# Performance work log

Measured on AMD Instinct MI355X. Metric: run time of the kernel, lower is better.

## Reference

```python
import math
import jax, jax.numpy as jnp
import numpy as np

B, N, D = 32, 1025, 768
K, CD, TD = 64, 128, 256  # num_clusters, cluster_dim, token_dim
REG = 0.1
NUM_ITERS = 5


def setup_inputs() -> dict:
    key = jax.random.key(0)
    ks = jax.random.split(key, 8)
    x = jax.random.normal(ks[0], (B, N, D), dtype=jnp.float32)
    # Linear params (torch nn.Linear: y = x @ W.T + b; we store W already transposed as [in, out])
    Wf = jax.random.normal(ks[1], (D, CD), dtype=jnp.float32) / math.sqrt(D)
    bf = jnp.zeros((CD,), dtype=jnp.float32)
    Ws = jax.random.normal(ks[2], (D, K), dtype=jnp.float32) / math.sqrt(D)
    bs = jnp.zeros((K,), dtype=jnp.float32)
    Wt = jax.random.normal(ks[3], (D, TD), dtype=jnp.float32) / math.sqrt(D)
    bt = jnp.zeros((TD,), dtype=jnp.float32)
    anchors = jax.random.normal(ks[4], (K, CD), dtype=jnp.float32) * 0.1
    dust_bin = jnp.float32(1.0)
    sharpness = jnp.float32(5.0)
    return {"x": x, "Wf": Wf, "bf": bf, "Ws": Ws, "bs": bs, "Wt": Wt, "bt": bt,
            "anchors": anchors, "dust_bin": dust_bin, "sharpness": sharpness}


def _log_otp_solver(log_a, log_b, M, num_iters, reg):
    M = M / reg
    u = jnp.zeros_like(log_a)  # [B, K+1]
    v = jnp.zeros_like(log_b)  # [B, N-1]
    for _ in range(num_iters):
        u = log_a - jax.nn.logsumexp(M + v[:, None, :], axis=2)
        v = log_b - jax.nn.logsumexp(M + u[:, :, None], axis=1)
    return M + u[:, :, None] + v[:, None, :]


def reference(x, Wf, bf, Ws, bs, Wt, bt, anchors, dust_bin, sharpness):
    b, n, d = x.shape
    t_global = x[:, 0]            # [B, D]
    fi = x[:, 1:]                 # [B, N-1, D]
    f = fi @ Wf + bf              # [B, N-1, CD]
    s = jnp.swapaxes(fi @ Ws + bs, 1, 2)  # [B, K, N-1]
    t = t_global @ Wt + bt        # [B, TD]
    s = s * sharpness
    dust = jnp.broadcast_to(dust_bin, (b, 1, n - 1))
    s_aug = jnp.concatenate([s, dust], axis=1)  # [B, K+1, N-1]
    log_a = jnp.full((b, K + 1), -math.log(K + 1), dtype=x.dtype)
    log_b = jnp.full((b, n - 1), -math.log(n - 1), dtype=x.dtype)
    log_P = _log_otp_solver(log_a, log_b, s_aug, NUM_ITERS, REG)
    p = jnp.exp(log_P)[:, :-1, :]  # [B, K, N-1]
    # v_agg = sum_n p[b,k,n] * (2*f[b,n,:] - anchors[k,:])  (algebraic rewrite of the broadcast sum)
    v_agg = 2.0 * jnp.einsum('bkn,bnc->bkc', p, f) - p.sum(axis=2)[:, :, None] * anchors[None]
    v_local = v_agg.reshape(b, -1)            # [B, K*CD]
    f_out = jnp.concatenate([t, v_local], axis=-1)
    norm = jnp.maximum(jnp.linalg.norm(f_out, axis=-1, keepdims=True), 1e-12)
    return f_out / norm
```

## Files before the change

kernel.cpp:

```cpp
#include <hip/hip_runtime.h>
#include <math.h>


#define BATCH 32
#define NTOK  1025
#define DIM   768
#define KDIM  64
#define CDIM  128
#define TDIM  256
#define NM1   1024
#define ROWLEN 8448
#define NITER 5
#define INV_REG 10.0f
#define NS_AGG 8
#define LOG_A (-4.17438727f)
#define LOG_B (-6.93147181f)

typedef __attribute__((ext_vector_type(8))) short short8;
typedef __attribute__((ext_vector_type(4))) float floatx4;

typedef __attribute__((address_space(3))) unsigned int lds_uint;
typedef const __attribute__((address_space(1))) unsigned int glb_uint;

__device__ __forceinline__ void gload_lds16(const void* g, void* l) {
    __builtin_amdgcn_global_load_lds((glb_uint*)g, (lds_uint*)l, 16, 0, 0);
}

__device__ __forceinline__ unsigned short bf16_rne(float f) {
    unsigned u = __builtin_bit_cast(unsigned, f);
    unsigned r = u + 0x7FFFu + ((u >> 16) & 1u);
    return (unsigned short)(r >> 16);
}

__device__ __forceinline__ short8 cvt8(float4 a, float4 b) {
    short8 r;
    r[0] = (short)bf16_rne(a.x); r[1] = (short)bf16_rne(a.y);
    r[2] = (short)bf16_rne(a.z); r[3] = (short)bf16_rne(a.w);
    r[4] = (short)bf16_rne(b.x); r[5] = (short)bf16_rne(b.y);
    r[6] = (short)bf16_rne(b.z); r[7] = (short)bf16_rne(b.w);
    return r;
}

__global__ __launch_bounds__(256) void prep(
    const float* __restrict__ Wf, const float* __restrict__ Ws,
    const float* __restrict__ bf, const float* __restrict__ bs,
    const float* __restrict__ x, const float* __restrict__ Wt,
    short* __restrict__ W_pack, float* __restrict__ bias_all,
    float* __restrict__ tpart)
{
    __shared__ float xr[256];
    const int blk = blockIdx.x, tid = threadIdx.x;
    if (blk < 576) {
        int idx = blk * 256 + tid;
        int g    = idx / 6144;
        int rem  = idx - g * 6144;
        int nf   = rem >> 9;
        int rem2 = rem & 511;
        int lane = rem2 >> 3;
        int j    = rem2 & 7;
        int k = g * 32 + (lane >> 4) * 8 + j;
        int c = nf * 16 + (lane & 15);
        float v = (c < CDIM) ? Wf[(size_t)k * CDIM + c] : Ws[(size_t)k * KDIM + (c - CDIM)];
        W_pack[idx] = (short)bf16_rne(v);
        if (idx < 192) bias_all[idx] = (idx < CDIM) ? bf[idx] : bs[idx - CDIM];
    } else {
        int i = blk - 576;
        int b = i / 3, dy = i - b * 3;
        xr[tid] = x[(size_t)b * NTOK * DIM + (size_t)dy * 256 + tid];
        __syncthreads();
        float acc = 0.f;
        const float* wp = Wt + (size_t)dy * 256 * TDIM + tid;
#pragma unroll 8
        for (int d = 0; d < 256; ++d) acc = fmaf(xr[d], wp[(size_t)d * TDIM], acc);
        tpart[((size_t)dy * BATCH + b) * TDIM + tid] = acc;
    }
}

__global__ __launch_bounds__(256, 2) void gemm_fs(
    const float* __restrict__ x, const short* __restrict__ W_pack,
    const float* __restrict__ bias_all, const float* __restrict__ sharp_p,
    unsigned short* __restrict__ fT, float* __restrict__ Mmat)
{
    __shared__ __align__(16) short Bs[12288];
    __shared__ __align__(16) short As[4096];
    const int tid  = threadIdx.x;
    const int wave = tid >> 6, lane = tid & 63;
    const int quad = lane >> 4, lrow = lane & 15;
    const int bb0   = blockIdx.x & 31;
    const int chunk = blockIdx.x >> 5;
    const int R = bb0 * 1024 + chunk * 64 + wave * 16;

    const int arow = bb0 * 1024 + chunk * 64 + (tid >> 2);
    const float* asrc = x + ((size_t)(arow >> 10) * NTOK + 1 + (arow & 1023)) * DIM + (tid & 3) * 16;
    const int r    = (tid >> 2) & 15;
    const int seg  = tid & 3;
    const int kk_w = seg >> 1;
    const int q0   = (seg & 1) * 2;
    short* adst0 = &As[(((tid >> 6) * 2 + kk_w) * 64 + q0 * 16 + r) * 8];
    short* adst1 = &As[(((tid >> 6) * 2 + kk_w) * 64 + (q0 + 1) * 16 + r) * 8];

    floatx4 acc[12];
#pragma unroll
    for (int nf = 0; nf < 12; ++nf) acc[nf] = (floatx4){0.f, 0.f, 0.f, 0.f};

    float4 g0 = *(const float4*)(asrc);
    float4 g1 = *(const float4*)(asrc + 4);
    float4 g2 = *(const float4*)(asrc + 8);
    float4 g3 = *(const float4*)(asrc + 12);

    for (int ko = 0; ko < 12; ++ko) {
        __syncthreads();
        const short* bsrc = W_pack + ko * 12288 + tid * 8;
#pragma unroll
        for (int i = 0; i < 6; ++i)
            gload_lds16(bsrc + i * 2048, &Bs[i * 2048 + tid * 8]);
        *(short8*)adst0 = cvt8(g0, g1);
        *(short8*)adst1 = cvt8(g2, g3);
        __syncthreads();
        if (ko < 11) {
            const float* ap = asrc + (ko + 1) * 64;
            g0 = *(const float4*)(ap);
            g1 = *(const float4*)(ap + 4);
            g2 = *(const float4*)(ap + 8);
            g3 = *(const float4*)(ap + 12);
            __builtin_amdgcn_sched_barrier(0);
        }
#pragma unroll
        for (int kk = 0; kk < 2; ++kk) {
            short8 af = *(const short8*)&As[((wave * 2 + kk) * 64 + lane) * 8];
#pragma unroll
            for (int nf = 0; nf < 12; ++nf) {
                short8 bf8 = *(const short8*)&Bs[((kk * 12 + nf) * 64 + lane) * 8];
                acc[nf] = __builtin_amdgcn_mfma_f32_16x16x32_bf16(af, bf8, acc[nf], 0, 0, 0);
            }
        }
    }

    const float sc = sharp_p[0] * INV_REG;
    const int bb = R >> 10;
    const int tok = (R & 1023) + quad * 4;
#pragma unroll
    for (int nf = 0; nf < 12; ++nf) {
        const int c = nf * 16 + lrow;
        const float bias = bias_all[c];
        if (nf < 8) {
            ushort4 w;
            w.x = bf16_rne(acc[nf][0] + bias);
            w.y = bf16_rne(acc[nf][1] + bias);
            w.z = bf16_rne(acc[nf][2] + bias);
            w.w = bf16_rne(acc[nf][3] + bias);
            *(ushort4*)(fT + ((size_t)bb * CDIM + c) * NM1 + tok) = w;
        } else {
            const int k = c - CDIM;
            float4 w = make_float4((acc[nf][0] + bias) * sc, (acc[nf][1] + bias) * sc,
                                   (acc[nf][2] + bias) * sc, (acc[nf][3] + bias) * sc);
            *(float4*)(Mmat + ((size_t)bb * KDIM + k) * NM1 + tok) = w;
        }
    }
}

template<bool FIRST>
__global__ __launch_bounds__(256) void sink_u(
    const float* __restrict__ Mmat, const float* __restrict__ v_in,
    const float* __restrict__ dust_p, float* __restrict__ u_out)
{
    const int b   = blockIdx.x & 31;
    const int sub = blockIdx.x >> 5;
    const int k   = sub * 4 + (threadIdx.x >> 6);
    if (k > 64) return;
    const int lane = threadIdx.x & 63;
    const float dustM = dust_p[0] * INV_REG;

    const float4* vp = (const float4*)(v_in + (size_t)b * NM1);
    float xs[16];
    if (k < 64) {
        const float4* Mp = (const float4*)(Mmat + ((size_t)b * KDIM + k) * NM1);
#pragma unroll
        for (int i = 0; i < 4; ++i) {
            float4 mv = Mp[i * 64 + lane];
            float4 vv = FIRST ? make_float4(0.f, 0.f, 0.f, 0.f) : vp[i * 64 + lane];
            xs[i * 4 + 0] = mv.x + vv.x;
            xs[i * 4 + 1] = mv.y + vv.y;
            xs[i * 4 + 2] = mv.z + vv.z;
            xs[i * 4 + 3] = mv.w + vv.w;
        }
    } else {
#pragma unroll
        for (int i = 0; i < 4; ++i) {
            float4 vv = FIRST ? make_float4(0.f, 0.f, 0.f, 0.f) : vp[i * 64 + lane];
            xs[i * 4 + 0] = dustM + vv.x;
            xs[i * 4 + 1] = dustM + vv.y;
            xs[i * 4 + 2] = dustM + vv.z;
            xs[i * 4 + 3] = dustM + vv.w;
        }
    }
    float m = xs[0];
#pragma unroll
    for (int i = 1; i < 16; ++i) m = fmaxf(m, xs[i]);
#pragma unroll
    for (int off = 1; off < 64; off <<= 1) m = fmaxf(m, __shfl_xor(m, off));
    float S = 0.f;
#pragma unroll
    for (int i = 0; i < 16; ++i) S += __expf(xs[i] - m);
#pragma unroll
    for (int off = 1; off < 64; off <<= 1) S += __shfl_xor(S, off);
    if (lane == 0) u_out[b * 65 + k] = LOG_A - (m + __logf(S));
}

__global__ __launch_bounds__(256) void sink_v(
    const float* __restrict__ Mmat, const float* __restrict__ u_in,
    const float* __restrict__ dust_p, float* __restrict__ v_out)
{
    __shared__ float us[65];
    __shared__ float2 pp[4][64];
    const int b   = blockIdx.x & 31;
    const int ns2 = blockIdx.x >> 5;
    const int tid = threadIdx.x;
    const int tok = tid & 63, kq = tid >> 6;
    const int n = ns2 * 64 + tok;
    if (tid < 65) us[tid] = u_in[b * 65 + tid];
    __syncthreads();
    const float* Mb = Mmat + ((size_t)b * KDIM + kq * 16) * NM1 + n;
    float xs[16];
#pragma unroll
    for (int kk = 0; kk < 16; ++kk) xs[kk] = Mb[(size_t)kk * NM1] + us[kq * 16 + kk];
    float m = xs[0];
#pragma unroll
    for (int kk = 1; kk < 16; ++kk) m = fmaxf(m, xs[kk]);
    float e = 0.f;
#pragma unroll
    for (int kk = 0; kk < 16; ++kk) e += __expf(xs[kk] - m);
    pp[kq][tok] = make_float2(m, e);
    __syncthreads();
    if (tid < 64) {
        const float xd = dust_p[0] * INV_REG + us[64];
        float m3 = xd;
#pragma unroll
        for (int q = 0; q < 4; ++q) m3 = fmaxf(m3, pp[q][tid].x);
        float S3 = __expf(xd - m3);
#pragma unroll
        for (int q = 0; q < 4; ++q) S3 += pp[q][tid].y * __expf(pp[q][tid].x - m3);
        v_out[(size_t)b * NM1 + ns2 * 64 + tid] = LOG_B - (m3 + __logf(S3));
    }
}

__global__ __launch_bounds__(256) void aggregate(
    const float* __restrict__ Mmat, const unsigned short* __restrict__ fT,
    const float* __restrict__ u_in, const float* __restrict__ dust_p,
    float* __restrict__ vpart, float* __restrict__ rspart)
{
    __shared__ float us[65];
    __shared__ __align__(16) float vsh[128];
    __shared__ float wv[4][128][2];
    const int b = blockIdx.x, ns = blockIdx.y;
    const int tid = threadIdx.x;
    const int wave = tid >> 6, lane = tid & 63;
    const int quad = lane >> 4, lrow = lane & 15;
    const int krow = wave * 16 + lrow;
    const float dustM = dust_p[0] * INV_REG;

    if (tid < 65) us[tid] = u_in[b * 65 + tid];
    __syncthreads();

    float mreg[32];
    {
        const float* Mrow = Mmat + ((size_t)b * KDIM + krow) * NM1 + ns * 128 + quad * 8;
#pragma unroll
        for (int s = 0; s < 4; ++s) {
            float4 a = *(const float4*)(Mrow + s * 32);
            float4 c = *(const float4*)(Mrow + s * 32 + 4);
            mreg[s*8+0]=a.x; mreg[s*8+1]=a.y; mreg[s*8+2]=a.z; mreg[s*8+3]=a.w;
            mreg[s*8+4]=c.x; mreg[s*8+5]=c.y; mreg[s*8+6]=c.z; mreg[s*8+7]=c.w;
        }
    }

    const float uk = us[krow];
#pragma unroll
    for (int s = 0; s < 4; ++s) {
#pragma unroll
        for (int j = 0; j < 8; ++j) {
            float x = mreg[s*8+j] + uk;
            float m2 = x;
            m2 = fmaxf(m2, __shfl_xor(m2, 1));
            m2 = fmaxf(m2, __shfl_xor(m2, 2));
            m2 = fmaxf(m2, __shfl_xor(m2, 4));
            m2 = fmaxf(m2, __shfl_xor(m2, 8));
            float e = __expf(x - m2);
            e += __shfl_xor(e, 1);
            e += __shfl_xor(e, 2);
            e += __shfl_xor(e, 4);
            e += __shfl_xor(e, 8);
            if (lrow == 0) {
                wv[wave][s*32 + quad*8 + j][0] = m2;
                wv[wave][s*32 + quad*8 + j][1] = e;
            }
        }
    }
    __syncthreads();
    if (tid < 128) {
        const float xd = dustM + us[64];
        float m3 = xd;
#pragma unroll
        for (int w = 0; w < 4; ++w) m3 = fmaxf(m3, wv[w][tid][0]);
        float S3 = __expf(xd - m3);
#pragma unroll
        for (int w = 0; w < 4; ++w) S3 += wv[w][tid][1] * __expf(wv[w][tid][0] - m3);
        vsh[tid] = LOG_B - (m3 + __logf(S3));
    }
    __syncthreads();

    const unsigned short* fbase = fT + ((size_t)b * CDIM + lrow) * NM1 + ns * 128 + quad * 8;
    floatx4 acc[8];
#pragma unroll
    for (int nf = 0; nf < 8; ++nf) acc[nf] = (floatx4){0.f, 0.f, 0.f, 0.f};
    float rs = 0.f;
#pragma unroll
    for (int s = 0; s < 4; ++s) {
        const int tb = s * 32 + quad * 8;
        float4 v0 = *(const float4*)&vsh[tb];
        float4 v1 = *(const float4*)&vsh[tb + 4];
        float p[8];
        p[0] = __expf(mreg[s*8+0] + uk + v0.x);
        p[1] = __expf(mreg[s*8+1] + uk + v0.y);
        p[2] = __expf(mreg[s*8+2] + uk + v0.z);
        p[3] = __expf(mreg[s*8+3] + uk + v0.w);
        p[4] = __expf(mreg[s*8+4] + uk + v1.x);
        p[5] = __expf(mreg[s*8+5] + uk + v1.y);
        p[6] = __expf(mreg[s*8+6] + uk + v1.z);
        p[7] = __expf(mreg[s*8+7] + uk + v1.w);
        short8 afrag;
#pragma unroll
        for (int j = 0; j < 8; ++j) {
            rs += p[j];
            afrag[j] = (short)bf16_rne(p[j]);
        }
#pragma unroll
        for (int nf = 0; nf < 8; ++nf) {
            short8 bfrag = *(const short8*)(fbase + (size_t)nf * 16 * NM1 + s * 32);
            acc[nf] = __builtin_amdgcn_mfma_f32_16x16x32_bf16(afrag, bfrag, acc[nf], 0, 0, 0);
        }
    }
    rs += __shfl_xor(rs, 16);
    rs += __shfl_xor(rs, 32);
    if (lane < 16) rspart[(ns * BATCH + b) * KDIM + krow] = rs;

    float* vp = vpart + (size_t)(ns * BATCH + b) * (KDIM * CDIM);
#pragma unroll
    for (int nf = 0; nf < 8; ++nf) {
        const int c = nf * 16 + lrow;
#pragma unroll
        for (int j = 0; j < 4; ++j)
            vp[(size_t)(wave * 16 + quad * 4 + j) * CDIM + c] = acc[nf][j];
    }
}

__global__ __launch_bounds__(1024) void finalize_all(
    const float* __restrict__ vpart, const float* __restrict__ rspart,
    const float* __restrict__ anchors, const float* __restrict__ tpart,
    const float* __restrict__ bt, float* __restrict__ out)
{
    __shared__ float rstot[KDIM];
    __shared__ float red[16];
    __shared__ float sc_sh;
    const int b = blockIdx.x, tid = threadIdx.x;
    const int lane = tid & 63, wave = tid >> 6;

    if (tid < KDIM) {
        float s = 0.f;
#pragma unroll
        for (int ns = 0; ns < NS_AGG; ++ns)
            s += rspart[(ns * BATCH + b) * KDIM + tid];
        rstot[tid] = s;
    }
    __syncthreads();

    const size_t e0 = (size_t)tid * 8;
    float4 s0 = make_float4(0.f, 0.f, 0.f, 0.f);
    float4 s1 = make_float4(0.f, 0.f, 0.f, 0.f);
#pragma unroll
    for (int ns = 0; ns < NS_AGG; ++ns) {
        const float* vp = vpart + (size_t)(ns * BATCH + b) * (KDIM * CDIM) + e0;
        float4 a = *(const float4*)(vp);
        float4 c = *(const float4*)(vp + 4);
        s0.x += a.x; s0.y += a.y; s0.z += a.z; s0.w += a.w;
        s1.x += c.x; s1.y += c.y; s1.z += c.z; s1.w += c.w;
    }
    const float rsv = rstot[tid >> 4];
    float4 a0 = *(const float4*)(anchors + e0);
    float4 a1 = *(const float4*)(anchors + e0 + 4);
    float4 v0, v1;
    v0.x = 2.f * s0.x - rsv * a0.x;  v0.y = 2.f * s0.y - rsv * a0.y;
    v0.z = 2.f * s0.z - rsv * a0.z;  v0.w = 2.f * s0.w - rsv * a0.w;
    v1.x = 2.f * s1.x - rsv * a1.x;  v1.y = 2.f * s1.y - rsv * a1.y;
    v1.z = 2.f * s1.z - rsv * a1.z;  v1.w = 2.f * s1.w - rsv * a1.w;
    float ss = v0.x*v0.x + v0.y*v0.y + v0.z*v0.z + v0.w*v0.w
             + v1.x*v1.x + v1.y*v1.y + v1.z*v1.z + v1.w*v1.w;

    float t = 0.f;
    if (tid < TDIM) {
        t = bt[tid];
#pragma unroll
        for (int s = 0; s < 3; ++s) t += tpart[((size_t)s * BATCH + b) * TDIM + tid];
        ss += t * t;
    }

#pragma unroll
    for (int off = 32; off > 0; off >>= 1) ss += __shfl_down(ss, off);
    if (lane == 0) red[wave] = ss;
    __syncthreads();
    if (tid == 0) {
        float tot = 0.f;
#pragma unroll
        for (int i = 0; i < 16; ++i) tot += red[i];
        sc_sh = 1.f / fmaxf(sqrtf(tot), 1e-12f);
    }
    __syncthreads();
    const float scale = sc_sh;

    float* orow = out + (size_t)b * ROWLEN;
    if (tid < TDIM) orow[tid] = t * scale;
    v0.x *= scale; v0.y *= scale; v0.z *= scale; v0.w *= scale;
    v1.x *= scale; v1.y *= scale; v1.z *= scale; v1.w *= scale;
    *(float4*)&orow[TDIM + e0]     = v0;
    *(float4*)&orow[TDIM + e0 + 4] = v1;
}

extern "C" void kernel_launch(void* const* d_in, const int* in_sizes, int n_in,
                              void* d_out, int out_size, void* d_ws, size_t ws_size,
                              hipStream_t stream)
{
    const float* x       = (const float*)d_in[0];
    const float* Wf      = (const float*)d_in[1];
    const float* bf      = (const float*)d_in[2];
    const float* Ws      = (const float*)d_in[3];
    const float* bs      = (const float*)d_in[4];
    const float* Wt      = (const float*)d_in[5];
    const float* bt      = (const float*)d_in[6];
    const float* anchors = (const float*)d_in[7];
    const float* dust    = (const float*)d_in[8];
    const float* sharp   = (const float*)d_in[9];
    float* out = (float*)d_out;

    char* base = (char*)d_ws;
    short* W_pack        = (short*)base;
    float* bias_all      = (float*)(base + 294912);
    float* Mmat          = bias_all + 192;
    unsigned short* fT   = (unsigned short*)(Mmat + (size_t)BATCH * KDIM * NM1);
    float* u_buf         = (float*)(fT + (size_t)BATCH * CDIM * NM1);
    float* v_buf         = u_buf + BATCH * 65;
    float* vpart         = v_buf + BATCH * NM1;
    float* rspart        = vpart + (size_t)NS_AGG * BATCH * KDIM * CDIM;
    float* tpart         = rspart + NS_AGG * BATCH * KDIM;

    hipLaunchKernelGGL(prep, dim3(672), dim3(256), 0, stream,
                       Wf, Ws, bf, bs, x, Wt, W_pack, bias_all, tpart);
    hipLaunchKernelGGL(gemm_fs, dim3(512), dim3(256), 0, stream,
                       x, W_pack, bias_all, sharp, fT, Mmat);

    hipLaunchKernelGGL(HIP_KERNEL_NAME(sink_u<true>), dim3(544), dim3(256), 0, stream,
                       Mmat, v_buf, dust, u_buf);
    for (int it = 1; it < NITER; ++it) {
        hipLaunchKernelGGL(sink_v, dim3(512), dim3(256), 0, stream,
                           Mmat, u_buf, dust, v_buf);
        hipLaunchKernelGGL(HIP_KERNEL_NAME(sink_u<false>), dim3(544), dim3(256), 0, stream,
                           Mmat, v_buf, dust, u_buf);
    }

    hipLaunchKernelGGL(aggregate, dim3(BATCH, NS_AGG), dim3(256), 0, stream,
                       Mmat, fT, u_buf, dust, vpart, rspart);
    hipLaunchKernelGGL(finalize_all, dim3(BATCH), dim3(1024), 0, stream,
                       vpart, rspart, anchors, tpart, bt, out);
}
```

Before: 241.6 us.

## Fuse Sinkhorn v/u half-steps into one kernel and double-buffer GEMM tiles

Each Sinkhorn iteration after the first now runs as a single sink_uv kernel. It computes v for a 128-token slice and emits per-slice partial logsumexp statistics (max, sum) for the next u update. The consumer kernel (next sink_uv or aggregate) merges these eight partials into u, which removes the separate sink_u launch and its full re-read of Mmat. The GEMM stage also gets double-buffered LDS for A and B tiles, so the next K-chunk loads while MFMAs run, at the cost of twice the shared memory, which may lower occupancy.

```diff
diff --git a/kernel.cpp b/kernel.cpp
--- a/kernel.cpp
+++ b/kernel.cpp
@@ -81,8 +81,8 @@
     const float* __restrict__ bias_all, const float* __restrict__ sharp_p,
     unsigned short* __restrict__ fT, float* __restrict__ Mmat)
 {
-    __shared__ __align__(16) short Bs[12288];
-    __shared__ __align__(16) short As[4096];
+    __shared__ __align__(16) short Bs[2][12288];
+    __shared__ __align__(16) short As[2][4096];
     const int tid  = threadIdx.x;
     const int wave = tid >> 6, lane = tid & 63;
     const int quad = lane >> 4, lrow = lane & 15;
@@ -96,8 +96,8 @@
     const int seg  = tid & 3;
     const int kk_w = seg >> 1;
     const int q0   = (seg & 1) * 2;
-    short* adst0 = &As[(((tid >> 6) * 2 + kk_w) * 64 + q0 * 16 + r) * 8];
-    short* adst1 = &As[(((tid >> 6) * 2 + kk_w) * 64 + (q0 + 1) * 16 + r) * 8];
+    const int aoff0 = (((tid >> 6) * 2 + kk_w) * 64 + q0 * 16 + r) * 8;
+    const int aoff1 = (((tid >> 6) * 2 + kk_w) * 64 + (q0 + 1) * 16 + r) * 8;
 
     floatx4 acc[12];
 #pragma unroll
@@ -107,33 +107,51 @@
     float4 g1 = *(const float4*)(asrc + 4);
     float4 g2 = *(const float4*)(asrc + 8);
     float4 g3 = *(const float4*)(asrc + 12);
+    {
+        const short* bsrc = W_pack + tid * 8;
+#pragma unroll
+        for (int i = 0; i < 6; ++i)
+            gload_lds16(bsrc + i * 2048, &Bs[0][i * 2048 + tid * 8]);
+    }
+    *(short8*)&As[0][aoff0] = cvt8(g0, g1);
+    *(short8*)&As[0][aoff1] = cvt8(g2, g3);
+    {
+        const float* ap = asrc + 64;
+        g0 = *(const float4*)(ap);
+        g1 = *(const float4*)(ap + 4);
+        g2 = *(const float4*)(ap + 8);
+        g3 = *(const float4*)(ap + 12);
+    }
+    __syncthreads();
 
     for (int ko = 0; ko < 12; ++ko) {
-        __syncthreads();
-        const short* bsrc = W_pack + ko * 12288 + tid * 8;
-#pragma unroll
-        for (int i = 0; i < 6; ++i)
-            gload_lds16(bsrc + i * 2048, &Bs[i * 2048 + tid * 8]);
-        *(short8*)adst0 = cvt8(g0, g1);
-        *(short8*)adst1 = cvt8(g2, g3);
-        __syncthreads();
+        const int buf = ko & 1;
         if (ko < 11) {
-            const float* ap = asrc + (ko + 1) * 64;
-            g0 = *(const float4*)(ap);
-            g1 = *(const float4*)(ap + 4);
-            g2 = *(const float4*)(ap + 8);
-            g3 = *(const float4*)(ap + 12);
+            const short* bsrc = W_pack + (ko + 1) * 12288 + tid * 8;
+#pragma unroll
+            for (int i = 0; i < 6; ++i)
+                gload_lds16(bsrc + i * 2048, &Bs[buf ^ 1][i * 2048 + tid * 8]);
+            *(short8*)&As[buf ^ 1][aoff0] = cvt8(g0, g1);
+            *(short8*)&As[buf ^ 1][aoff1] = cvt8(g2, g3);
+            if (ko < 10) {
+                const float* ap = asrc + (ko + 2) * 64;
+                g0 = *(const float4*)(ap);
+                g1 = *(const float4*)(ap + 4);
+                g2 = *(const float4*)(ap + 8);
+                g3 = *(const float4*)(ap + 12);
+            }
             __builtin_amdgcn_sched_barrier(0);
         }
 #pragma unroll
         for (int kk = 0; kk < 2; ++kk) {
-            short8 af = *(const short8*)&As[((wave * 2 + kk) * 64 + lane) * 8];
+            short8 af = *(const short8*)&As[buf][((wave * 2 + kk) * 64 + lane) * 8];
 #pragma unroll
             for (int nf = 0; nf < 12; ++nf) {
-                short8 bf8 = *(const short8*)&Bs[((kk * 12 + nf) * 64 + lane) * 8];
+                short8 bf8 = *(const short8*)&Bs[buf][((kk * 12 + nf) * 64 + lane) * 8];
                 acc[nf] = __builtin_amdgcn_mfma_f32_16x16x32_bf16(af, bf8, acc[nf], 0, 0, 0);
             }
         }
+        __syncthreads();
     }
 
     const float sc = sharp_p[0] * INV_REG;
@@ -207,46 +225,101 @@
     if (lane == 0) u_out[b * 65 + k] = LOG_A - (m + __logf(S));
 }
 
-__global__ __launch_bounds__(256) void sink_v(
-    const float* __restrict__ Mmat, const float* __restrict__ u_in,
-    const float* __restrict__ dust_p, float* __restrict__ v_out)
+template<bool UPART>
+__global__ __launch_bounds__(256) void sink_uv(
+    const float* __restrict__ Mmat, const float* __restrict__ dust_p,
+    const float* __restrict__ u_direct, const float2* __restrict__ pin,
+    float2* __restrict__ pout)
 {
     __shared__ float us[65];
-    __shared__ float2 pp[4][64];
-    const int b   = blockIdx.x & 31;
-    const int ns2 = blockIdx.x >> 5;
+    __shared__ float2 xch[2][128];
+    __shared__ float2 wvp[4][32];
+    __shared__ float2 dsh[2];
+    const int b = blockIdx.x & 31, ns = blockIdx.x >> 5;
     const int tid = threadIdx.x;
-    const int tok = tid & 63, kq = tid >> 6;
-    const int n = ns2 * 64 + tok;
-    if (tid < 65) us[tid] = u_in[b * 65 + tid];
-    __syncthreads();
-    const float* Mb = Mmat + ((size_t)b * KDIM + kq * 16) * NM1 + n;
-    float xs[16];
-#pragma unroll
-    for (int kk = 0; kk < 16; ++kk) xs[kk] = Mb[(size_t)kk * NM1] + us[kq * 16 + kk];
-    float m = xs[0];
-#pragma unroll
-    for (int kk = 1; kk < 16; ++kk) m = fmaxf(m, xs[kk]);
-    float e = 0.f;
-#pragma unroll
-    for (int kk = 0; kk < 16; ++kk) e += __expf(xs[kk] - m);
-    pp[kq][tok] = make_float2(m, e);
-    __syncthreads();
-    if (tid < 64) {
-        const float xd = dust_p[0] * INV_REG + us[64];
-        float m3 = xd;
-#pragma unroll
-        for (int q = 0; q < 4; ++q) m3 = fmaxf(m3, pp[q][tid].x);
-        float S3 = __expf(xd - m3);
-#pragma unroll
-        for (int q = 0; q < 4; ++q) S3 += pp[q][tid].y * __expf(pp[q][tid].x - m3);
-        v_out[(size_t)b * NM1 + ns2 * 64 + tid] = LOG_B - (m3 + __logf(S3));
+    const int tn = tid & 127;
+    const int kh = tid >> 7;
+    const int lane = tid & 63, wave = tid >> 6;
+    const float dustM = dust_p[0] * INV_REG;
+
+    float mreg[32];
+    const float* Mb = Mmat + ((size_t)b * KDIM + kh * 32) * NM1 + ns * 128 + tn;
+#pragma unroll
+    for (int i = 0; i < 32; ++i) mreg[i] = Mb[(size_t)i * NM1];
+
+    if (tid < 65) {
+        if (UPART) {
+            const float2* pr = pin + (size_t)b * NS_AGG * 65 + tid;
+            float2 pv[8];
+            float M2 = -3.4e38f;
+#pragma unroll
+            for (int q = 0; q < 8; ++q) { pv[q] = pr[q * 65]; M2 = fmaxf(M2, pv[q].x); }
+            float S2 = 0.f;
+#pragma unroll
+            for (int q = 0; q < 8; ++q) S2 += pv[q].y * __expf(pv[q].x - M2);
+            us[tid] = LOG_A - (M2 + __logf(S2));
+        } else {
+            us[tid] = u_direct[b * 65 + tid];
+        }
+    }
+    __syncthreads();
+
+    float mm = mreg[0] + us[kh * 32];
+#pragma unroll
+    for (int i = 1; i < 32; ++i) mm = fmaxf(mm, mreg[i] + us[kh * 32 + i]);
+    float ee = 0.f;
+#pragma unroll
+    for (int i = 0; i < 32; ++i) ee += __expf(mreg[i] + us[kh * 32 + i] - mm);
+    xch[kh][tn] = make_float2(mm, ee);
+    __syncthreads();
+    float2 a0 = xch[0][tn], a1 = xch[1][tn];
+    const float xd = dustM + us[64];
+    float m3 = fmaxf(fmaxf(a0.x, a1.x), xd);
+    float S3 = a0.y * __expf(a0.x - m3) + a1.y * __expf(a1.x - m3) + __expf(xd - m3);
+    const float v = LOG_B - (m3 + __logf(S3));
+
+    float rmx = 0.f, re = 0.f;
+#pragma unroll
+    for (int i = 0; i < 32; ++i) {
+        float xv = mreg[i] + v;
+        float mx = xv;
+#pragma unroll
+        for (int off = 1; off < 64; off <<= 1) mx = fmaxf(mx, __shfl_xor(mx, off));
+        float e = __expf(xv - mx);
+#pragma unroll
+        for (int off = 1; off < 64; off <<= 1) e += __shfl_xor(e, off);
+        if (lane == i) { rmx = mx; re = e; }
+    }
+    if (lane < 32) wvp[wave][lane] = make_float2(rmx, re);
+    if (kh == 0) {
+        float mv = v;
+#pragma unroll
+        for (int off = 1; off < 64; off <<= 1) mv = fmaxf(mv, __shfl_xor(mv, off));
+        float ev = __expf(v - mv);
+#pragma unroll
+        for (int off = 1; off < 64; off <<= 1) ev += __shfl_xor(ev, off);
+        if (lane == 0) dsh[wave] = make_float2(mv, ev);
+    }
+    __syncthreads();
+    if (tid < 65) {
+        float2 o;
+        if (tid < 64) {
+            const int w0 = (tid >> 5) * 2, i = tid & 31;
+            float2 p0 = wvp[w0][i], p1 = wvp[w0 + 1][i];
+            float m = fmaxf(p0.x, p1.x);
+            o = make_float2(m, p0.y * __expf(p0.x - m) + p1.y * __expf(p1.x - m));
+        } else {
+            float2 d0 = dsh[0], d1 = dsh[1];
+            float m = fmaxf(d0.x, d1.x);
+            o = make_float2(dustM + m, d0.y * __expf(d0.x - m) + d1.y * __expf(d1.x - m));
+        }
+        pout[((size_t)b * NS_AGG + ns) * 65 + tid] = o;
     }
 }
 
 __global__ __launch_bounds__(256) void aggregate(
     const float* __restrict__ Mmat, const unsigned short* __restrict__ fT,
-    const float* __restrict__ u_in, const float* __restrict__ dust_p,
+    const float2* __restrict__ pin, const float* __restrict__ dust_p,
     float* __restrict__ vpart, float* __restrict__ rspart)
 {
     __shared__ float us[65];
@@ -259,7 +332,17 @@
     const int krow = wave * 16 + lrow;
     const float dustM = dust_p[0] * INV_REG;
 
-    if (tid < 65) us[tid] = u_in[b * 65 + tid];
+    if (tid < 65) {
+        const float2* pr = pin + (size_t)b * NS_AGG * 65 + tid;
+        float2 pv[8];
+        float M2 = -3.4e38f;
+#pragma unroll
+        for (int q = 0; q < 8; ++q) { pv[q] = pr[q * 65]; M2 = fmaxf(M2, pv[q].x); }
+        float S2 = 0.f;
+#pragma unroll
+        for (int q = 0; q < 8; ++q) S2 += pv[q].y * __expf(pv[q].x - M2);
+        us[tid] = LOG_A - (M2 + __logf(S2));
+    }
     __syncthreads();
 
     float mreg[32];
@@ -279,13 +362,13 @@
     for (int s = 0; s < 4; ++s) {
 #pragma unroll
         for (int j = 0; j < 8; ++j) {
-            float x = mreg[s*8+j] + uk;
-            float m2 = x;
+            float xv = mreg[s*8+j] + uk;
+            float m2 = xv;
             m2 = fmaxf(m2, __shfl_xor(m2, 1));
             m2 = fmaxf(m2, __shfl_xor(m2, 2));
             m2 = fmaxf(m2, __shfl_xor(m2, 4));
             m2 = fmaxf(m2, __shfl_xor(m2, 8));
-            float e = __expf(x - m2);
+            float e = __expf(xv - m2);
             e += __shfl_xor(e, 1);
             e += __shfl_xor(e, 2);
             e += __shfl_xor(e, 4);
@@ -447,8 +530,9 @@
     float* Mmat          = bias_all + 192;
     unsigned short* fT   = (unsigned short*)(Mmat + (size_t)BATCH * KDIM * NM1);
     float* u_buf         = (float*)(fT + (size_t)BATCH * CDIM * NM1);
-    float* v_buf         = u_buf + BATCH * 65;
-    float* vpart         = v_buf + BATCH * NM1;
+    float2* partA        = (float2*)(u_buf + BATCH * 65);
+    float2* partB        = partA + (size_t)BATCH * NS_AGG * 65;
+    float* vpart         = (float*)(partB + (size_t)BATCH * NS_AGG * 65);
     float* rspart        = vpart + (size_t)NS_AGG * BATCH * KDIM * CDIM;
     float* tpart         = rspart + NS_AGG * BATCH * KDIM;
 
@@ -458,16 +542,18 @@
                        x, W_pack, bias_all, sharp, fT, Mmat);
 
     hipLaunchKernelGGL(HIP_KERNEL_NAME(sink_u<true>), dim3(544), dim3(256), 0, stream,
-                       Mmat, v_buf, dust, u_buf);
-    for (int it = 1; it < NITER; ++it) {
-        hipLaunchKernelGGL(sink_v, dim3(512), dim3(256), 0, stream,
-                           Mmat, u_buf, dust, v_buf);
-        hipLaunchKernelGGL(HIP_KERNEL_NAME(sink_u<false>), dim3(544), dim3(256), 0, stream,
-                           Mmat, v_buf, dust, u_buf);
-    }
+                       Mmat, u_buf, dust, u_buf);
+    hipLaunchKernelGGL(HIP_KERNEL_NAME(sink_uv<false>), dim3(256), dim3(256), 0, stream,
+                       Mmat, dust, u_buf, partA, partA);
+    hipLaunchKernelGGL(HIP_KERNEL_NAME(sink_uv<true>), dim3(256), dim3(256), 0, stream,
+                       Mmat, dust, u_buf, partA, partB);
+    hipLaunchKernelGGL(HIP_KERNEL_NAME(sink_uv<true>), dim3(256), dim3(256), 0, stream,
+                       Mmat, dust, u_buf, partB, partA);
+    hipLaunchKernelGGL(HIP_KERNEL_NAME(sink_uv<true>), dim3(256), dim3(256), 0, stream,
+                       Mmat, dust, u_buf, partA, partB);
 
     hipLaunchKernelGGL(aggregate, dim3(BATCH, NS_AGG), dim3(256), 0, stream,
-                       Mmat, fT, u_buf, dust, vpart, rspart);
+                       Mmat, fT, partB, dust, vpart, rspart);
     hipLaunchKernelGGL(finalize_all, dim3(BATCH), dim3(1024), 0, stream,
                        vpart, rspart, anchors, tpart, bt, out);
 }
```

Measured after the change: 255.0 us. 1.06x slower.

## Double-buffer LDS tiles in gemm_fs to overlap loads with MFMA

Applied to the files above, without the earlier changes.

Splits the A and B shared-memory tiles in the fused projection GEMM into two buffers. The next k-slice is loaded into the alternate buffer while MFMAs run on the current one, which cuts the two barriers per iteration down to one. The cost is double the LDS use (about 64KB per block), which can limit occupancy under launch_bounds(256,2). The global-to-LDS direct loads may also still need waits before the barrier.

```diff
diff --git a/kernel.cpp b/kernel.cpp
--- a/kernel.cpp
+++ b/kernel.cpp
@@ -81,8 +81,8 @@
     const float* __restrict__ bias_all, const float* __restrict__ sharp_p,
     unsigned short* __restrict__ fT, float* __restrict__ Mmat)
 {
-    __shared__ __align__(16) short Bs[12288];
-    __shared__ __align__(16) short As[4096];
+    __shared__ __align__(16) short Bs[2][12288];
+    __shared__ __align__(16) short As[2][4096];
     const int tid  = threadIdx.x;
     const int wave = tid >> 6, lane = tid & 63;
     const int quad = lane >> 4, lrow = lane & 15;
@@ -96,8 +96,8 @@
     const int seg  = tid & 3;
     const int kk_w = seg >> 1;
     const int q0   = (seg & 1) * 2;
-    short* adst0 = &As[(((tid >> 6) * 2 + kk_w) * 64 + q0 * 16 + r) * 8];
-    short* adst1 = &As[(((tid >> 6) * 2 + kk_w) * 64 + (q0 + 1) * 16 + r) * 8];
+    const int aoff0 = (((tid >> 6) * 2 + kk_w) * 64 + q0 * 16 + r) * 8;
+    const int aoff1 = (((tid >> 6) * 2 + kk_w) * 64 + (q0 + 1) * 16 + r) * 8;
 
     floatx4 acc[12];
 #pragma unroll
@@ -107,33 +107,51 @@
     float4 g1 = *(const float4*)(asrc + 4);
     float4 g2 = *(const float4*)(asrc + 8);
     float4 g3 = *(const float4*)(asrc + 12);
+    {
+        const short* bsrc = W_pack + tid * 8;
+#pragma unroll
+        for (int i = 0; i < 6; ++i)
+            gload_lds16(bsrc + i * 2048, &Bs[0][i * 2048 + tid * 8]);
+    }
+    *(short8*)&As[0][aoff0] = cvt8(g0, g1);
+    *(short8*)&As[0][aoff1] = cvt8(g2, g3);
+    {
+        const float* ap = asrc + 64;
+        g0 = *(const float4*)(ap);
+        g1 = *(const float4*)(ap + 4);
+        g2 = *(const float4*)(ap + 8);
+        g3 = *(const float4*)(ap + 12);
+    }
+    __syncthreads();
 
     for (int ko = 0; ko < 12; ++ko) {
-        __syncthreads();
-        const short* bsrc = W_pack + ko * 12288 + tid * 8;
-#pragma unroll
-        for (int i = 0; i < 6; ++i)
-            gload_lds16(bsrc + i * 2048, &Bs[i * 2048 + tid * 8]);
-        *(short8*)adst0 = cvt8(g0, g1);
-        *(short8*)adst1 = cvt8(g2, g3);
-        __syncthreads();
+        const int buf = ko & 1;
         if (ko < 11) {
-            const float* ap = asrc + (ko + 1) * 64;
-            g0 = *(const float4*)(ap);
-            g1 = *(const float4*)(ap + 4);
-            g2 = *(const float4*)(ap + 8);
-            g3 = *(const float4*)(ap + 12);
+            const short* bsrc = W_pack + (ko + 1) * 12288 + tid * 8;
+#pragma unroll
+            for (int i = 0; i < 6; ++i)
+                gload_lds16(bsrc + i * 2048, &Bs[buf ^ 1][i * 2048 + tid * 8]);
+            *(short8*)&As[buf ^ 1][aoff0] = cvt8(g0, g1);
+            *(short8*)&As[buf ^ 1][aoff1] = cvt8(g2, g3);
+            if (ko < 10) {
+                const float* ap = asrc + (ko + 2) * 64;
+                g0 = *(const float4*)(ap);
+                g1 = *(const float4*)(ap + 4);
+                g2 = *(const float4*)(ap + 8);
+                g3 = *(const float4*)(ap + 12);
+            }
             __builtin_amdgcn_sched_barrier(0);
         }
 #pragma unroll
         for (int kk = 0; kk < 2; ++kk) {
-            short8 af = *(const short8*)&As[((wave * 2 + kk) * 64 + lane) * 8];
+            short8 af = *(const short8*)&As[buf][((wave * 2 + kk) * 64 + lane) * 8];
 #pragma unroll
             for (int nf = 0; nf < 12; ++nf) {
-                short8 bf8 = *(const short8*)&Bs[((kk * 12 + nf) * 64 + lane) * 8];
+                short8 bf8 = *(const short8*)&Bs[buf][((kk * 12 + nf) * 64 + lane) * 8];
                 acc[nf] = __builtin_amdgcn_mfma_f32_16x16x32_bf16(af, bf8, acc[nf], 0, 0, 0);
             }
         }
+        __syncthreads();
     }
 
     const float sc = sharp_p[0] * INV_REG;
```

After: 242.8 us. No clear change (+0.5%).

## Fuse first Sinkhorn u-update into the GEMM epilogue via partial logsumexp

Applied to the files above, without the earlier changes.

The GEMM epilogue now computes per-chunk max and sum-exp partials for each cluster row, plus a constant partial for the dust row, and writes them to a small buffer. The first sink_v pass combines the 16 chunk partials into u, so the standalone first sink_u launch and its full read of Mmat go away. The iteration loop is reordered to keep the same sequence of u and v updates. In exchange, the GEMM epilogue gains shuffles, exp calls and an extra barrier.

```diff
diff --git a/kernel.cpp b/kernel.cpp
--- a/kernel.cpp
+++ b/kernel.cpp
@@ -79,10 +79,13 @@
 __global__ __launch_bounds__(256, 2) void gemm_fs(
     const float* __restrict__ x, const short* __restrict__ W_pack,
     const float* __restrict__ bias_all, const float* __restrict__ sharp_p,
-    unsigned short* __restrict__ fT, float* __restrict__ Mmat)
+    const float* __restrict__ dust_p,
+    unsigned short* __restrict__ fT, float* __restrict__ Mmat,
+    float2* __restrict__ part0)
 {
     __shared__ __align__(16) short Bs[12288];
     __shared__ __align__(16) short As[4096];
+    __shared__ float2 sm[4][4][16];
     const int tid  = threadIdx.x;
     const int wave = tid >> 6, lane = tid & 63;
     const int quad = lane >> 4, lrow = lane & 15;
@@ -137,6 +140,7 @@
     }
 
     const float sc = sharp_p[0] * INV_REG;
+    const float dustM = dust_p[0] * INV_REG;
     const int bb = R >> 10;
     const int tok = (R & 1023) + quad * 4;
 #pragma unroll
@@ -155,11 +159,35 @@
             float4 w = make_float4((acc[nf][0] + bias) * sc, (acc[nf][1] + bias) * sc,
                                    (acc[nf][2] + bias) * sc, (acc[nf][3] + bias) * sc);
             *(float4*)(Mmat + ((size_t)bb * KDIM + k) * NM1 + tok) = w;
-        }
-    }
-}
-
-template<bool FIRST>
+            float m = fmaxf(fmaxf(w.x, w.y), fmaxf(w.z, w.w));
+            m = fmaxf(m, __shfl_xor(m, 16));
+            m = fmaxf(m, __shfl_xor(m, 32));
+            float e = __expf(w.x - m) + __expf(w.y - m)
+                    + __expf(w.z - m) + __expf(w.w - m);
+            e += __shfl_xor(e, 16);
+            e += __shfl_xor(e, 32);
+            if (quad == 0) sm[wave][nf - 8][lrow] = make_float2(m, e);
+        }
+    }
+    __syncthreads();
+    if (tid < 65) {
+        float2 o;
+        if (tid < 64) {
+            float2 p0 = sm[0][tid >> 4][tid & 15];
+            float2 p1 = sm[1][tid >> 4][tid & 15];
+            float2 p2 = sm[2][tid >> 4][tid & 15];
+            float2 p3 = sm[3][tid >> 4][tid & 15];
+            float m = fmaxf(fmaxf(p0.x, p1.x), fmaxf(p2.x, p3.x));
+            float e = p0.y * __expf(p0.x - m) + p1.y * __expf(p1.x - m)
+                    + p2.y * __expf(p2.x - m) + p3.y * __expf(p3.x - m);
+            o = make_float2(m, e);
+        } else {
+            o = make_float2(dustM, 64.f);
+        }
+        part0[((size_t)bb0 * 16 + chunk) * 65 + tid] = o;
+    }
+}
+
 __global__ __launch_bounds__(256) void sink_u(
     const float* __restrict__ Mmat, const float* __restrict__ v_in,
     const float* __restrict__ dust_p, float* __restrict__ u_out)
@@ -178,7 +206,7 @@
 #pragma unroll
         for (int i = 0; i < 4; ++i) {
             float4 mv = Mp[i * 64 + lane];
-            float4 vv = FIRST ? make_float4(0.f, 0.f, 0.f, 0.f) : vp[i * 64 + lane];
+            float4 vv = vp[i * 64 + lane];
             xs[i * 4 + 0] = mv.x + vv.x;
             xs[i * 4 + 1] = mv.y + vv.y;
             xs[i * 4 + 2] = mv.z + vv.z;
@@ -187,7 +215,7 @@
     } else {
 #pragma unroll
         for (int i = 0; i < 4; ++i) {
-            float4 vv = FIRST ? make_float4(0.f, 0.f, 0.f, 0.f) : vp[i * 64 + lane];
+            float4 vv = vp[i * 64 + lane];
             xs[i * 4 + 0] = dustM + vv.x;
             xs[i * 4 + 1] = dustM + vv.y;
             xs[i * 4 + 2] = dustM + vv.z;
@@ -207,8 +235,10 @@
     if (lane == 0) u_out[b * 65 + k] = LOG_A - (m + __logf(S));
 }
 
+template<bool UPART>
 __global__ __launch_bounds__(256) void sink_v(
     const float* __restrict__ Mmat, const float* __restrict__ u_in,
+    const float2* __restrict__ part0,
     const float* __restrict__ dust_p, float* __restrict__ v_out)
 {
     __shared__ float us[65];
@@ -218,7 +248,21 @@
     const int tid = threadIdx.x;
     const int tok = tid & 63, kq = tid >> 6;
     const int n = ns2 * 64 + tok;
-    if (tid < 65) us[tid] = u_in[b * 65 + tid];
+    if (tid < 65) {
+        if (UPART) {
+            const float2* pr = part0 + (size_t)b * 16 * 65 + tid;
+            float M2 = -3.4e38f;
+            float2 pv[16];
+#pragma unroll
+            for (int q = 0; q < 16; ++q) { pv[q] = pr[q * 65]; M2 = fmaxf(M2, pv[q].x); }
+            float S2 = 0.f;
+#pragma unroll
+            for (int q = 0; q < 16; ++q) S2 += pv[q].y * __expf(pv[q].x - M2);
+            us[tid] = LOG_A - (M2 + __logf(S2));
+        } else {
+            us[tid] = u_in[b * 65 + tid];
+        }
+    }
     __syncthreads();
     const float* Mb = Mmat + ((size_t)b * KDIM + kq * 16) * NM1 + n;
     float xs[16];
@@ -448,22 +492,24 @@
     unsigned short* fT   = (unsigned short*)(Mmat + (size_t)BATCH * KDIM * NM1);
     float* u_buf         = (float*)(fT + (size_t)BATCH * CDIM * NM1);
     float* v_buf         = u_buf + BATCH * 65;
-    float* vpart         = v_buf + BATCH * NM1;
+    float2* part0        = (float2*)(v_buf + BATCH * NM1);
+    float* vpart         = (float*)(part0 + (size_t)BATCH * 16 * 65);
     float* rspart        = vpart + (size_t)NS_AGG * BATCH * KDIM * CDIM;
     float* tpart         = rspart + NS_AGG * BATCH * KDIM;
 
     hipLaunchKernelGGL(prep, dim3(672), dim3(256), 0, stream,
                        Wf, Ws, bf, bs, x, Wt, W_pack, bias_all, tpart);
     hipLaunchKernelGGL(gemm_fs, dim3(512), dim3(256), 0, stream,
-                       x, W_pack, bias_all, sharp, fT, Mmat);
-
-    hipLaunchKernelGGL(HIP_KERNEL_NAME(sink_u<true>), dim3(544), dim3(256), 0, stream,
-                       Mmat, v_buf, dust, u_buf);
+                       x, W_pack, bias_all, sharp, dust, fT, Mmat, part0);
+
+    hipLaunchKernelGGL(HIP_KERNEL_NAME(sink_v<true>), dim3(512), dim3(256), 0, stream,
+                       Mmat, u_buf, part0, dust, v_buf);
     for (int it = 1; it < NITER; ++it) {
-        hipLaunchKernelGGL(sink_v, dim3(512), dim3(256), 0, stream,
-                           Mmat, u_buf, dust, v_buf);
-        hipLaunchKernelGGL(HIP_KERNEL_NAME(sink_u<false>), dim3(544), dim3(256), 0, stream,
+        hipLaunchKernelGGL(sink_u, dim3(544), dim3(256), 0, stream,
                            Mmat, v_buf, dust, u_buf);
+        if (it < NITER - 1)
+            hipLaunchKernelGGL(HIP_KERNEL_NAME(sink_v<false>), dim3(512), dim3(256), 0, stream,
+                               Mmat, u_buf, part0, dust, v_buf);
     }
 
     hipLaunchKernelGGL(aggregate, dim3(BATCH, NS_AGG), dim3(256), 0, stream,
```

Result: no change. 238.6 us (-1.2%).
